# Kernel optimization log

Measured on AMD Instinct MI355X. Metric: run time of the kernel, lower is better.

Reference implementation:

```python
import jax, jax.numpy as jnp
import numpy as np
import heapq
from collections import defaultdict

V = 50257   # vocab_size
D = 512     # embedding_dim
B = 4096    # batch of (embedding, target) samples


def _build_paths(freqs):
    """Huffman tree exactly as in HierarchicalSoftmax.build_tree; returns padded path arrays."""
    heap = [[w, [n]] for n, w in freqs.items()]
    heapq.heapify(heap)
    tree = defaultdict(list)
    while len(heap) > 1:
        lo = heapq.heappop(heap)
        hi = heapq.heappop(heap)
        for node in lo[1]:
            tree[node].append((len(heap), 0))
        for node in hi[1]:
            tree[node].append((len(heap), 1))
        heapq.heappush(heap, [lo[0] + hi[0], lo[1] + hi[1]])
    n_leaves = len(freqs)
    L = max(len(tree[v]) for v in range(n_leaves))  # max path length (~27 for zipf)
    nodes = np.zeros((n_leaves, L), dtype=np.int32)
    dirs = np.zeros((n_leaves, L), dtype=np.int32)
    mask = np.zeros((n_leaves, L), dtype=bool)
    for v in range(n_leaves):
        for i, (p, d) in enumerate(tree[v]):
            nodes[v, i] = p
            dirs[v, i] = d
            mask[v, i] = True
    return nodes, dirs, mask


def setup_inputs() -> dict:
    key = jax.random.key(0)
    k1, k2, k3 = jax.random.split(key, 3)
    freqs = {i: 1.0 / (i + 1) for i in range(V)}  # deterministic zipf frequencies
    nodes, dirs, mask = _build_paths(freqs)
    embeddings = jax.random.normal(k1, (B, D), dtype=jnp.float32)
    # one Linear(D,1) per internal node: V-1 internal nodes total
    W = jax.random.normal(k2, (V - 1, D), dtype=jnp.float32) * (1.0 / np.sqrt(D))
    b = jnp.zeros((V - 1,), dtype=jnp.float32)
    target = jax.random.randint(k3, (B,), 0, V)
    return {
        "embeddings": embeddings,
        "W": W,
        "b": b,
        "target": target,
        "path_nodes": jnp.asarray(nodes),
        "path_dirs": jnp.asarray(dirs),
        "path_mask": jnp.asarray(mask),
    }


def reference(embeddings, W, b, target, path_nodes, path_dirs, path_mask):
    # Gather each sample's root-to-leaf path of internal-node classifiers.
    nodes = path_nodes[target]          # [B, L]
    dirs = path_dirs[target]            # [B, L]
    mask = path_mask[target]            # [B, L] bool
    Wg = W[nodes]                       # [B, L, D] gathered classifier rows
    scores = jnp.einsum('bld,bd->bl', Wg, embeddings) + b[nodes]  # [B, L]
    # direction==1 -> sigmoid(s); direction==0 -> 1 - sigmoid(s) == sigmoid(-s)
    signed = jnp.where(dirs == 1, scores, -scores)
    factors = jnp.where(mask, jax.nn.sigmoid(signed), 1.0)
    return jnp.prod(factors, axis=-1)   # [B] path probabilities
```

## Files before the change

kernel.cpp:

```cpp
#include <hip/hip_runtime.h>


#define HS_D 512
#define F4PL 8

__device__ __forceinline__ float fast_sigmoid(float s) {
    return __builtin_amdgcn_rcpf(1.0f + __expf(-s));
}

__device__ __forceinline__ float dot32(const float4* __restrict__ e,
                                       const float4* __restrict__ a) {
    float p = e[0].x * a[0].x;
    #pragma unroll
    for (int k = 0; k < F4PL; ++k) {
        if (k) p = fmaf(e[k].x, a[k].x, p);
        p = fmaf(e[k].y, a[k].y, p);
        p = fmaf(e[k].z, a[k].z, p);
        p = fmaf(e[k].w, a[k].w, p);
    }
    return p;
}

__global__ __launch_bounds__(256) void hs_kernel(
    const float* __restrict__ emb,
    const float* __restrict__ W,
    const float* __restrict__ bias,
    const int*   __restrict__ target,
    const int*   __restrict__ nodes,
    const int*   __restrict__ dirs,
    float*       __restrict__ out,
    int B, int L)
{
    const int b    = blockIdx.x;
    const int wv   = threadIdx.x >> 6;
    const int lane = threadIdx.x & 63;
    const int g    = lane >> 4;
    const int gl   = lane & 15;

    __shared__ float wprod[4];

    const int t = __builtin_amdgcn_readfirstlane(target[b]);

    int nval = 0, dval = 0;
    if (lane < L) {
        nval = nodes[(size_t)t * L + lane];
        dval = dirs [(size_t)t * L + lane];
    }
    const unsigned long long rootmask = __ballot(lane < L && nval == 0);
    const int plen = __ffsll((long long)rootmask);
    const unsigned long long dirmask = __ballot(dval != 0);

    const float4* e4 = (const float4*)(emb + (size_t)b * HS_D);
    float4 ek[F4PL];
    #pragma unroll
    for (int k = 0; k < F4PL; ++k) ek[k] = e4[gl + 16 * k];

    const int l0 = wv + 4 * g;
    const int l1 = l0 + 16;
    const int n0 = __shfl(nval, l0, 64);
    const int n1 = __shfl(nval, l1, 64);
    const bool act0 = (l0 < plen);
    const bool act1 = (l1 < plen);

    float lprod = 1.0f;

    float4 a1[F4PL];
    if (act1) {
        const float4* w4 = (const float4*)(W + (size_t)n1 * HS_D);
        #pragma unroll
        for (int k = 0; k < F4PL; ++k) a1[k] = w4[gl + 16 * k];
    }

    if (act0) {
        const float4* w4 = (const float4*)(W + (size_t)n0 * HS_D);
        float4 a0[F4PL];
        #pragma unroll
        for (int k = 0; k < F4PL; ++k) a0[k] = w4[gl + 16 * k];
        const float bi = bias[n0];
        float p = dot32(ek, a0);
        #pragma unroll
        for (int m = 8; m >= 1; m >>= 1) p += __shfl_xor(p, m, 64);
        float s = p + bi;
        s = ((dirmask >> l0) & 1ull) ? s : -s;
        lprod = fast_sigmoid(s);
    }

    if (act1) {
        const float bi = bias[n1];
        float p = dot32(ek, a1);
        #pragma unroll
        for (int m = 8; m >= 1; m >>= 1) p += __shfl_xor(p, m, 64);
        float s = p + bi;
        s = ((dirmask >> l1) & 1ull) ? s : -s;
        lprod *= fast_sigmoid(s);
    }

    for (int base = wv + 32; base < plen; base += 16) {
        const int l  = base + 4 * g;
        const int ls = (l < 64) ? l : 0;
        const int n  = __shfl(nval, ls, 64);
        if (l < plen) {
            const float4* w4 = (const float4*)(W + (size_t)n * HS_D);
            float4 a[F4PL];
            #pragma unroll
            for (int k = 0; k < F4PL; ++k) a[k] = w4[gl + 16 * k];
            float p = dot32(ek, a);
            #pragma unroll
            for (int m = 8; m >= 1; m >>= 1) p += __shfl_xor(p, m, 64);
            float s = p + bias[n];
            s = ((dirmask >> l) & 1ull) ? s : -s;
            lprod *= fast_sigmoid(s);
        }
    }

    lprod *= __shfl_xor(lprod, 16, 64);
    lprod *= __shfl_xor(lprod, 32, 64);

    if (lane == 0) wprod[wv] = lprod;
    __syncthreads();
    if (threadIdx.x == 0)
        out[b] = wprod[0] * wprod[1] * wprod[2] * wprod[3];
}

extern "C" void kernel_launch(void* const* d_in, const int* in_sizes, int n_in,
                              void* d_out, int out_size, void* d_ws, size_t ws_size,
                              hipStream_t stream)
{
    const float* emb    = (const float*)d_in[0];
    const float* W      = (const float*)d_in[1];
    const float* bias   = (const float*)d_in[2];
    const int*   target = (const int*)  d_in[3];
    const int*   nodes  = (const int*)  d_in[4];
    const int*   dirs   = (const int*)  d_in[5];
    float*       out    = (float*)d_out;

    const int B = in_sizes[3];
    const int V = in_sizes[2] + 1;
    const int L = in_sizes[4] / V;

    hs_kernel<<<B, 256, 0, stream>>>(emb, W, bias, target, nodes, dirs, out, B, L);
}
```

Before: 168.5 us.

## Map one wavefront per sample with double-buffered classifier row prefetch

Each wavefront now handles a whole sample instead of splitting one sample across four waves of a block, which removes the shared-memory reduction and __syncthreads. Within the wave, four 16-lane groups walk the path with a ping-pong register prefetch of the next W row, and the biases are loaded once per lane and shuffled. The catch is less parallelism per sample, so each wave runs a longer serial loop of about seven iterations. Register pressure also rises from the two buffers under the tighter launch bound.

```diff
diff --git a/kernel.cpp b/kernel.cpp
--- a/kernel.cpp
+++ b/kernel.cpp
@@ -21,7 +21,15 @@
     return p;
 }
 
-__global__ __launch_bounds__(256) void hs_kernel(
+__device__ __forceinline__ void loadrow(float4* __restrict__ dst,
+                                        const float* __restrict__ W,
+                                        int n, int gl) {
+    const float4* w4 = (const float4*)(W + (size_t)n * HS_D);
+    #pragma unroll
+    for (int k = 0; k < F4PL; ++k) dst[k] = w4[gl + 16 * k];
+}
+
+__global__ __launch_bounds__(256, 4) void hs_kernel(
     const float* __restrict__ emb,
     const float* __restrict__ W,
     const float* __restrict__ bias,
@@ -31,95 +39,68 @@
     float*       __restrict__ out,
     int B, int L)
 {
-    const int b    = blockIdx.x;
-    const int wv   = threadIdx.x >> 6;
+    const int wid  = blockIdx.x * (blockDim.x >> 6) + (threadIdx.x >> 6);
     const int lane = threadIdx.x & 63;
     const int g    = lane >> 4;
     const int gl   = lane & 15;
+    if (wid >= B) return;
 
-    __shared__ float wprod[4];
+    const float4* e4 = (const float4*)(emb + (size_t)wid * HS_D);
+    float4 ek[F4PL];
+    #pragma unroll
+    for (int k = 0; k < F4PL; ++k) ek[k] = e4[gl + 16 * k];
 
-    const int t = __builtin_amdgcn_readfirstlane(target[b]);
+    const int t = __builtin_amdgcn_readfirstlane(target[wid]);
 
     int nval = 0, dval = 0;
+    float bval = 0.0f;
     if (lane < L) {
         nval = nodes[(size_t)t * L + lane];
         dval = dirs [(size_t)t * L + lane];
+        bval = bias[nval];
     }
     const unsigned long long rootmask = __ballot(lane < L && nval == 0);
     const int plen = __ffsll((long long)rootmask);
     const unsigned long long dirmask = __ballot(dval != 0);
 
-    const float4* e4 = (const float4*)(emb + (size_t)b * HS_D);
-    float4 ek[F4PL];
-    #pragma unroll
-    for (int k = 0; k < F4PL; ++k) ek[k] = e4[gl + 16 * k];
+    float lprod = 1.0f;
+    float4 bufA[F4PL], bufB[F4PL];
 
-    const int l0 = wv + 4 * g;
-    const int l1 = l0 + 16;
-    const int n0 = __shfl(nval, l0, 64);
-    const int n1 = __shfl(nval, l1, 64);
-    const bool act0 = (l0 < plen);
-    const bool act1 = (l1 < plen);
+    int l = g;
+    if (l < plen) loadrow(bufA, W, __shfl(nval, l, 64), gl);
 
-    float lprod = 1.0f;
-
-    float4 a1[F4PL];
-    if (act1) {
-        const float4* w4 = (const float4*)(W + (size_t)n1 * HS_D);
-        #pragma unroll
-        for (int k = 0; k < F4PL; ++k) a1[k] = w4[gl + 16 * k];
-    }
-
-    if (act0) {
-        const float4* w4 = (const float4*)(W + (size_t)n0 * HS_D);
-        float4 a0[F4PL];
-        #pragma unroll
-        for (int k = 0; k < F4PL; ++k) a0[k] = w4[gl + 16 * k];
-        const float bi = bias[n0];
-        float p = dot32(ek, a0);
-        #pragma unroll
-        for (int m = 8; m >= 1; m >>= 1) p += __shfl_xor(p, m, 64);
-        float s = p + bi;
-        s = ((dirmask >> l0) & 1ull) ? s : -s;
-        lprod = fast_sigmoid(s);
-    }
-
-    if (act1) {
-        const float bi = bias[n1];
-        float p = dot32(ek, a1);
-        #pragma unroll
-        for (int m = 8; m >= 1; m >>= 1) p += __shfl_xor(p, m, 64);
-        float s = p + bi;
-        s = ((dirmask >> l1) & 1ull) ? s : -s;
-        lprod *= fast_sigmoid(s);
-    }
-
-    for (int base = wv + 32; base < plen; base += 16) {
-        const int l  = base + 4 * g;
-        const int ls = (l < 64) ? l : 0;
-        const int n  = __shfl(nval, ls, 64);
-        if (l < plen) {
-            const float4* w4 = (const float4*)(W + (size_t)n * HS_D);
-            float4 a[F4PL];
-            #pragma unroll
-            for (int k = 0; k < F4PL; ++k) a[k] = w4[gl + 16 * k];
-            float p = dot32(ek, a);
+    while (l < plen) {
+        {
+            const int l2 = l + 4;
+            if (l2 < plen) loadrow(bufB, W, __shfl(nval, l2 & 63, 64), gl);
+            const float bi = __shfl(bval, l, 64);
+            float p = dot32(ek, bufA);
             #pragma unroll
             for (int m = 8; m >= 1; m >>= 1) p += __shfl_xor(p, m, 64);
-            float s = p + bias[n];
+            float s = p + bi;
             s = ((dirmask >> l) & 1ull) ? s : -s;
             lprod *= fast_sigmoid(s);
+            l = l2;
+        }
+        if (l >= plen) break;
+        {
+            const int l2 = l + 4;
+            if (l2 < plen) loadrow(bufA, W, __shfl(nval, l2 & 63, 64), gl);
+            const float bi = __shfl(bval, l, 64);
+            float p = dot32(ek, bufB);
+            #pragma unroll
+            for (int m = 8; m >= 1; m >>= 1) p += __shfl_xor(p, m, 64);
+            float s = p + bi;
+            s = ((dirmask >> l) & 1ull) ? s : -s;
+            lprod *= fast_sigmoid(s);
+            l = l2;
         }
     }
 
     lprod *= __shfl_xor(lprod, 16, 64);
     lprod *= __shfl_xor(lprod, 32, 64);
 
-    if (lane == 0) wprod[wv] = lprod;
-    __syncthreads();
-    if (threadIdx.x == 0)
-        out[b] = wprod[0] * wprod[1] * wprod[2] * wprod[3];
+    if (lane == 0) out[wid] = lprod;
 }
 
 extern "C" void kernel_launch(void* const* d_in, const int* in_sizes, int n_in,
@@ -138,5 +119,7 @@
     const int V = in_sizes[2] + 1;
     const int L = in_sizes[4] / V;
 
-    hs_kernel<<<B, 256, 0, stream>>>(emb, W, bias, target, nodes, dirs, out, B, L);
+    const int wavesPerBlock = 4;
+    const int grid = (B + wavesPerBlock - 1) / wavesPerBlock;
+    hs_kernel<<<grid, 256, 0, stream>>>(emb, W, bias, target, nodes, dirs, out, B, L);
 }
```

After: 163.2 us. 3.1% less time.
